# Optimization experiments

Measured on AMD Instinct MI355X. Metric: run time of the kernel, lower is better.

The kernel has to match this reference:

```python
import jax, jax.numpy as jnp
import numpy as np

V, E, H, S = 50257, 1024, 1024, 2048


def setup_inputs() -> dict:
    key = jax.random.key(0)
    ks = jax.random.split(key, 24)
    def n(k, shape, s=0.02):
        return jax.random.normal(k, shape, dtype=jnp.float32) * s
    inp = {
        "x": jax.random.normal(ks[0], (1, E), dtype=jnp.float32),
        "encoder_outputs": jax.random.normal(ks[1], (S, 2 * H), dtype=jnp.float32),
        "sentence": jax.random.randint(ks[2], (S,), 0, V, dtype=jnp.int32).at[0].set(7),
        "prev_probs": jax.random.uniform(ks[3], (V + S,), dtype=jnp.float32),
        "h0": n(ks[4], (1, H), 1.0),
        "c0": n(ks[5], (1, H), 1.0),
        "attn_W": n(ks[6], (S, 2 * H)), "attn_b": jnp.zeros((S,), jnp.float32),
        "comb_W": n(ks[7], (H, 2 * H)), "comb_b": jnp.zeros((H,), jnp.float32),
        "Ws_W": n(ks[8], (H, 2 * H)), "Ws_b": jnp.zeros((H,), jnp.float32),
        "Wo_W": n(ks[9], (V, H)), "Wo_b": jnp.zeros((V,), jnp.float32),
        "Wc_W": n(ks[10], (H, 2 * H)), "Wc_b": jnp.zeros((H,), jnp.float32),
        "W_ih": n(ks[11], (4 * H, E + 2 * H)), "W_hh": n(ks[12], (4 * H, H)),
        "b_ih": jnp.zeros((4 * H,), jnp.float32), "b_hh": jnp.zeros((4 * H,), jnp.float32),
        "prev_word": 7,
    }
    return inp


def reference(x, encoder_outputs, sentence, prev_probs, h0, c0,
              attn_W, attn_b, comb_W, comb_b, Ws_W, Ws_b,
              Wo_W, Wo_b, Wc_W, Wc_b, W_ih, W_hh, b_ih, b_hh, prev_word):
    xe, h, c = x[0], h0[0], c0[0]            # [E], [H], [H]
    # attentive read: attention over encoder positions, then combine to [H]
    att_logits = jnp.concatenate([xe, h]) @ attn_W.T + attn_b      # [S]
    attn_w = jax.nn.softmax(att_logits)
    ctx = attn_w @ encoder_outputs                                 # [2H]
    attentive = ctx @ comb_W.T + comb_b                            # [H]
    # selective read (copy mechanism): positions where sentence == prev_word
    probs_c = prev_probs[V:]                                       # [S]
    rho = jnp.where(sentence == prev_word, probs_c, 0.0)
    rho = rho / (rho.sum() + 1e-9)
    selective = (rho @ encoder_outputs) @ Ws_W.T + Ws_b            # [H]
    # single LSTM step (PyTorch gate order i,f,g,o)
    lstm_in = jnp.concatenate([xe, selective, attentive])          # [E+2H]
    gates = lstm_in @ W_ih.T + b_ih + h @ W_hh.T + b_hh            # [4H]
    i, f, g, o = jnp.split(gates, 4)
    c1 = jax.nn.sigmoid(f) * c + jax.nn.sigmoid(i) * jnp.tanh(g)
    h1 = jax.nn.sigmoid(o) * jnp.tanh(c1)                          # [H]
    # generate + copy scores, joint softmax
    score_g = h1 @ Wo_W.T + Wo_b                                   # [V]
    score_c = jnp.tanh(encoder_outputs @ Wc_W.T + Wc_b) @ h1       # [S]
    probs = jax.nn.softmax(jnp.concatenate([score_g, score_c]))    # [V+S]
    return probs, h1[None, :], c1[None, :]
```

## Files before the change

kernel.cpp:

```cpp
#include <hip/hip_runtime.h>
#include <hip/hip_bf16.h>
#include <math.h>

#define VV 50257
#define EE 1024
#define HH 1024
#define SS 2048
#define VS (VV + SS)

#define OFF_LOGA   0
#define OFF_ATTW   2048
#define OFF_RHO    4096
#define OFF_CTX    6144
#define OFF_SEL    8192
#define OFF_LSTMIN 10240
#define OFF_GATES  13312
#define OFF_H1     17408
#define OFF_LOG    18432
#define OFF_MS     70784
#define OFF_LS     70912
#define OFF_G      71040
#define OFF_T0     71168
#define OFF_T1     (71168 + 2048*1024)

typedef __attribute__((ext_vector_type(8))) short bf16x8;
typedef __attribute__((ext_vector_type(4))) float f32x4;

__device__ inline float wave_reduce(float v) {
    #pragma unroll
    for (int off = 32; off > 0; off >>= 1) v += __shfl_down(v, off, 64);
    return v;
}

__device__ inline unsigned short f2bf(float f) {
    unsigned int u = __builtin_bit_cast(unsigned int, f);
    u += 0x7FFFu + ((u >> 16) & 1u);
    return (unsigned short)(u >> 16);
}

__global__ void k_attn_logits(const float* __restrict__ x, const float* __restrict__ h0,
                              const float* __restrict__ attn_W, const float* __restrict__ attn_b,
                              float* __restrict__ out) {
    int wave = (blockIdx.x * blockDim.x + threadIdx.x) >> 6;
    int lane = threadIdx.x & 63;
    if (wave >= SS) return;
    const float4* rp = (const float4*)(attn_W + (size_t)wave * 2048);
    float acc = 0.f;
    #pragma unroll
    for (int k = 0; k < 8; ++k) {
        int idx = lane + 64 * k;
        float4 w = rp[idx];
        int j = idx * 4;
        const float* cat = (j < 1024) ? (x + j) : (h0 + (j - 1024));
        acc += w.x * cat[0] + w.y * cat[1] + w.z * cat[2] + w.w * cat[3];
    }
    acc = wave_reduce(acc);
    if (lane == 0) out[wave] = acc + attn_b[wave];
}

__global__ void k_prep(const float* __restrict__ logits, const int* __restrict__ sentence,
                       const float* __restrict__ prev_probs, const int* __restrict__ prev_word,
                       const float* __restrict__ x,
                       float* __restrict__ attn_w, float* __restrict__ rho,
                       float* __restrict__ lstm_in, float* __restrict__ ctxsel) {
    __shared__ float red[256];
    int tid = threadIdx.x;
    for (int j = tid; j < 4096; j += 256) ctxsel[j] = 0.f;
    float m = -1e30f;
    for (int s = tid; s < SS; s += 256) m = fmaxf(m, logits[s]);
    red[tid] = m; __syncthreads();
    for (int o = 128; o > 0; o >>= 1) { if (tid < o) red[tid] = fmaxf(red[tid], red[tid + o]); __syncthreads(); }
    m = red[0]; __syncthreads();
    float sum = 0.f;
    for (int s = tid; s < SS; s += 256) sum += expf(logits[s] - m);
    red[tid] = sum; __syncthreads();
    for (int o = 128; o > 0; o >>= 1) { if (tid < o) red[tid] += red[tid + o]; __syncthreads(); }
    float inv = 1.f / red[0]; __syncthreads();
    for (int s = tid; s < SS; s += 256) attn_w[s] = expf(logits[s] - m) * inv;
    int pw = prev_word[0];
    float rsum = 0.f;
    for (int s = tid; s < SS; s += 256) rsum += (sentence[s] == pw) ? prev_probs[VV + s] : 0.f;
    red[tid] = rsum; __syncthreads();
    for (int o = 128; o > 0; o >>= 1) { if (tid < o) red[tid] += red[tid + o]; __syncthreads(); }
    float rinv = 1.f / (red[0] + 1e-9f); __syncthreads();
    for (int s = tid; s < SS; s += 256) rho[s] = ((sentence[s] == pw) ? prev_probs[VV + s] : 0.f) * rinv;
    for (int j = tid; j < EE; j += 256) lstm_in[j] = x[j];
}

__global__ void k_ctx(const float* __restrict__ enc, const float* __restrict__ attn_w,
                      const float* __restrict__ rho, float* __restrict__ ctx,
                      float* __restrict__ selctx) {
    int col4 = blockIdx.x * 256 + threadIdx.x;
    int s0 = blockIdx.y * 64;
    float4 a = {0.f, 0.f, 0.f, 0.f}, r = {0.f, 0.f, 0.f, 0.f};
    const float4* p = (const float4*)enc + (size_t)s0 * 512 + col4;
    #pragma unroll 4
    for (int i = 0; i < 64; ++i) {
        float4 v = p[(size_t)i * 512];
        float w = attn_w[s0 + i], q = rho[s0 + i];
        a.x += w * v.x; a.y += w * v.y; a.z += w * v.z; a.w += w * v.w;
        r.x += q * v.x; r.y += q * v.y; r.z += q * v.z; r.w += q * v.w;
    }
    int c = col4 * 4;
    atomicAdd(&ctx[c], a.x); atomicAdd(&ctx[c+1], a.y); atomicAdd(&ctx[c+2], a.z); atomicAdd(&ctx[c+3], a.w);
    atomicAdd(&selctx[c], r.x); atomicAdd(&selctx[c+1], r.y); atomicAdd(&selctx[c+2], r.z); atomicAdd(&selctx[c+3], r.w);
}

__global__ void k_comb(const float* __restrict__ ctx, const float* __restrict__ selctx,
                       const float* __restrict__ comb_W, const float* __restrict__ comb_b,
                       const float* __restrict__ Ws_W, const float* __restrict__ Ws_b,
                       float* __restrict__ lstm_in) {
    int wave = (blockIdx.x * blockDim.x + threadIdx.x) >> 6;
    int lane = threadIdx.x & 63;
    if (wave >= 2048) return;
    bool sel = wave >= 1024;
    int i = sel ? wave - 1024 : wave;
    const float4* rp = (const float4*)((sel ? Ws_W : comb_W) + (size_t)i * 2048);
    const float4* vp = (const float4*)(sel ? selctx : ctx);
    float acc = 0.f;
    #pragma unroll
    for (int k = 0; k < 8; ++k) {
        int idx = lane + 64 * k;
        float4 w = rp[idx]; float4 v = vp[idx];
        acc += w.x * v.x + w.y * v.y + w.z * v.z + w.w * v.w;
    }
    acc = wave_reduce(acc);
    if (lane == 0) lstm_in[sel ? (1024 + i) : (2048 + i)] = acc + (sel ? Ws_b[i] : comb_b[i]);
}

__global__ __launch_bounds__(256) void k_gates_gemm(
        const float* __restrict__ lstm_in, const float* __restrict__ h0,
        const float* __restrict__ W_ih, const float* __restrict__ W_hh,
        const float* __restrict__ b_ih, const float* __restrict__ b_hh,
        float* __restrict__ gates,
        const float* __restrict__ A,
        const float* __restrict__ B,
        float* __restrict__ T0, float* __restrict__ T1) {
    __shared__ unsigned short As[128 * 32];
    __shared__ unsigned short Bs[128 * 32];
    int tid = threadIdx.x;
    if (blockIdx.x < 1024) {
        int wave = (blockIdx.x * 256 + tid) >> 6;
        int lane = tid & 63;
        const float4* rp = (const float4*)(W_ih + (size_t)wave * 3072);
        const float4* vp = (const float4*)lstm_in;
        float acc = 0.f;
        #pragma unroll
        for (int k = 0; k < 12; ++k) {
            int idx = lane + 64 * k;
            float4 w = rp[idx]; float4 v = vp[idx];
            acc += w.x * v.x + w.y * v.y + w.z * v.z + w.w * v.w;
        }
        const float4* hp = (const float4*)(W_hh + (size_t)wave * 1024);
        const float4* h4 = (const float4*)h0;
        #pragma unroll
        for (int k = 0; k < 4; ++k) {
            int idx = lane + 64 * k;
            float4 w = hp[idx]; float4 v = h4[idx];
            acc += w.x * v.x + w.y * v.y + w.z * v.z + w.w * v.w;
        }
        acc = wave_reduce(acc);
        if (lane == 0) gates[wave] = acc + b_ih[wave] + b_hh[wave];
        return;
    }
    int gg = blockIdx.x - 1024;
    int sK = gg >> 7;
    int rem = gg & 127;
    int mbase = (rem >> 3) * 128;
    int nbase = (rem & 7) * 128;
    float* C = sK ? T1 : T0;
    int lane = tid & 63;
    int wid = tid >> 6;
    int wm = (wid >> 1) * 64;
    int wn = (wid & 1) * 64;
    int lrow = lane & 15;
    int lk = (lane >> 4) * 8;
    f32x4 acc[4][4] = {};
    int kbeg = sK * 1024;
    for (int k0 = kbeg; k0 < kbeg + 1024; k0 += 32) {
        #pragma unroll
        for (int i = 0; i < 4; ++i) {
            int fi = tid + 256 * i;
            int row = fi >> 3;
            int kg = fi & 7;
            float4 v = *(const float4*)(A + (size_t)(mbase + row) * 2048 + k0 + kg * 4);
            ushort4 a4 = { f2bf(v.x), f2bf(v.y), f2bf(v.z), f2bf(v.w) };
            *(ushort4*)(As + row * 32 + kg * 4) = a4;
            float4 w = *(const float4*)(B + (size_t)(nbase + row) * 2048 + k0 + kg * 4);
            ushort4 b4 = { f2bf(w.x), f2bf(w.y), f2bf(w.z), f2bf(w.w) };
            *(ushort4*)(Bs + row * 32 + kg * 4) = b4;
        }
        __syncthreads();
        bf16x8 af[4], bfr[4];
        #pragma unroll
        for (int t = 0; t < 4; ++t) {
            af[t]  = *(const bf16x8*)(As + (wm + t * 16 + lrow) * 32 + lk);
            bfr[t] = *(const bf16x8*)(Bs + (wn + t * 16 + lrow) * 32 + lk);
        }
        #pragma unroll
        for (int mt = 0; mt < 4; ++mt)
            #pragma unroll
            for (int nt = 0; nt < 4; ++nt)
                acc[mt][nt] = __builtin_amdgcn_mfma_f32_16x16x32_bf16(af[mt], bfr[nt], acc[mt][nt], 0, 0, 0);
        __syncthreads();
    }
    int crow0 = (lane >> 4) * 4;
    int ccol = lane & 15;
    #pragma unroll
    for (int mt = 0; mt < 4; ++mt)
        #pragma unroll
        for (int nt = 0; nt < 4; ++nt) {
            int col = nbase + wn + nt * 16 + ccol;
            #pragma unroll
            for (int r = 0; r < 4; ++r) {
                int row = mbase + wm + mt * 16 + crow0 + r;
                C[(size_t)row * 1024 + col] = acc[mt][nt][r];
            }
        }
}

__global__ void k_lstm(const float* __restrict__ gates, const float* __restrict__ c0,
                       float* __restrict__ out, float* __restrict__ h1ws) {
    int k = blockIdx.x * 256 + threadIdx.x;
    float ig = gates[k], fg = gates[1024 + k], gg = gates[2048 + k], og = gates[3072 + k];
    float si = 1.f / (1.f + expf(-ig));
    float sf = 1.f / (1.f + expf(-fg));
    float so = 1.f / (1.f + expf(-og));
    float c1 = sf * c0[k] + si * tanhf(gg);
    float h1 = so * tanhf(c1);
    out[VS + k] = h1;
    out[VS + 1024 + k] = c1;
    h1ws[k] = h1;
}

__global__ void k_scores(const float* __restrict__ Wo_W, const float* __restrict__ Wo_b,
                         const float* __restrict__ T0, const float* __restrict__ T1,
                         const float* __restrict__ Wc_b,
                         const float* __restrict__ h1, float* __restrict__ logits) {
    int wave = (blockIdx.x * blockDim.x + threadIdx.x) >> 6;
    int lane = threadIdx.x & 63;
    if (wave >= VS) return;
    const float4* hp = (const float4*)h1;
    float acc = 0.f;
    if (wave < VV) {
        const float4* rp = (const float4*)(Wo_W + (size_t)wave * 1024);
        #pragma unroll
        for (int k = 0; k < 4; ++k) {
            int idx = lane + 64 * k;
            float4 w = rp[idx]; float4 v = hp[idx];
            acc += w.x * v.x + w.y * v.y + w.z * v.z + w.w * v.w;
        }
        acc = wave_reduce(acc);
        if (lane == 0) logits[wave] = acc + Wo_b[wave];
    } else {
        int r = wave - VV;
        const float4* p0 = (const float4*)(T0 + (size_t)r * 1024);
        const float4* p1 = (const float4*)(T1 + (size_t)r * 1024);
        const float4* bp = (const float4*)Wc_b;
        #pragma unroll
        for (int k = 0; k < 4; ++k) {
            int idx = lane + 64 * k;
            float4 a0 = p0[idx]; float4 a1 = p1[idx]; float4 bb = bp[idx]; float4 v = hp[idx];
            acc += tanhf(a0.x + a1.x + bb.x) * v.x + tanhf(a0.y + a1.y + bb.y) * v.y
                 + tanhf(a0.z + a1.z + bb.z) * v.z + tanhf(a0.w + a1.w + bb.w) * v.w;
        }
        acc = wave_reduce(acc);
        if (lane == 0) logits[wave] = acc;
    }
}

__global__ void k_sm1(const float* __restrict__ logits, float* __restrict__ ms, float* __restrict__ ls) {
    __shared__ float rm[256], rl[256];
    int tid = threadIdx.x;
    float m = -1e30f, l = 0.f;
    for (int v = blockIdx.x * 256 + tid; v < VS; v += 128 * 256) {
        float x = logits[v];
        float nm = fmaxf(m, x);
        l = l * expf(m - nm) + expf(x - nm);
        m = nm;
    }
    rm[tid] = m; rl[tid] = l; __syncthreads();
    for (int o = 128; o > 0; o >>= 1) {
        if (tid < o) {
            float m2 = rm[tid + o], l2 = rl[tid + o];
            float nm = fmaxf(rm[tid], m2);
            rl[tid] = rl[tid] * expf(rm[tid] - nm) + l2 * expf(m2 - nm);
            rm[tid] = nm;
        }
        __syncthreads();
    }
    if (tid == 0) { ms[blockIdx.x] = rm[0]; ls[blockIdx.x] = rl[0]; }
}

__global__ void k_sm2(const float* __restrict__ ms, const float* __restrict__ ls, float* __restrict__ g) {
    __shared__ float rm[128], rl[128];
    int tid = threadIdx.x;
    rm[tid] = ms[tid]; rl[tid] = ls[tid]; __syncthreads();
    for (int o = 64; o > 0; o >>= 1) {
        if (tid < o) {
            float m2 = rm[tid + o], l2 = rl[tid + o];
            float nm = fmaxf(rm[tid], m2);
            rl[tid] = rl[tid] * expf(rm[tid] - nm) + l2 * expf(m2 - nm);
            rm[tid] = nm;
        }
        __syncthreads();
    }
    if (tid == 0) { g[0] = rm[0]; g[1] = 1.f / rl[0]; }
}

__global__ void k_sm3(const float* __restrict__ logits, const float* __restrict__ g,
                      float* __restrict__ out) {
    int v = blockIdx.x * 256 + threadIdx.x;
    if (v < VS) out[v] = expf(logits[v] - g[0]) * g[1];
}

extern "C" void kernel_launch(void* const* d_in, const int* in_sizes, int n_in,
                              void* d_out, int out_size, void* d_ws, size_t ws_size,
                              hipStream_t stream) {
    (void)in_sizes; (void)n_in; (void)out_size; (void)ws_size;
    const float* x          = (const float*)d_in[0];
    const float* enc        = (const float*)d_in[1];
    const int*   sentence   = (const int*)d_in[2];
    const float* prev_probs = (const float*)d_in[3];
    const float* h0         = (const float*)d_in[4];
    const float* c0         = (const float*)d_in[5];
    const float* attn_W     = (const float*)d_in[6];
    const float* attn_b     = (const float*)d_in[7];
    const float* comb_W     = (const float*)d_in[8];
    const float* comb_b     = (const float*)d_in[9];
    const float* Ws_W       = (const float*)d_in[10];
    const float* Ws_b       = (const float*)d_in[11];
    const float* Wo_W       = (const float*)d_in[12];
    const float* Wo_b       = (const float*)d_in[13];
    const float* Wc_W       = (const float*)d_in[14];
    const float* Wc_b       = (const float*)d_in[15];
    const float* W_ih       = (const float*)d_in[16];
    const float* W_hh       = (const float*)d_in[17];
    const float* b_ih       = (const float*)d_in[18];
    const float* b_hh       = (const float*)d_in[19];
    const int*   prev_word  = (const int*)d_in[20];
    float* ws  = (float*)d_ws;
    float* out = (float*)d_out;

    k_attn_logits<<<512, 256, 0, stream>>>(x, h0, attn_W, attn_b, ws + OFF_LOGA);
    k_prep<<<1, 256, 0, stream>>>(ws + OFF_LOGA, sentence, prev_probs, prev_word, x,
                                  ws + OFF_ATTW, ws + OFF_RHO, ws + OFF_LSTMIN, ws + OFF_CTX);
    k_ctx<<<dim3(2, 32), 256, 0, stream>>>(enc, ws + OFF_ATTW, ws + OFF_RHO,
                                           ws + OFF_CTX, ws + OFF_SEL);
    k_comb<<<512, 256, 0, stream>>>(ws + OFF_CTX, ws + OFF_SEL, comb_W, comb_b,
                                    Ws_W, Ws_b, ws + OFF_LSTMIN);
    k_gates_gemm<<<1280, 256, 0, stream>>>(ws + OFF_LSTMIN, h0, W_ih, W_hh, b_ih, b_hh,
                                           ws + OFF_GATES, enc, Wc_W,
                                           ws + OFF_T0, ws + OFF_T1);
    k_lstm<<<4, 256, 0, stream>>>(ws + OFF_GATES, c0, out, ws + OFF_H1);
    k_scores<<<13077, 256, 0, stream>>>(Wo_W, Wo_b, ws + OFF_T0, ws + OFF_T1, Wc_b,
                                        ws + OFF_H1, ws + OFF_LOG);
    k_sm1<<<128, 256, 0, stream>>>(ws + OFF_LOG, ws + OFF_MS, ws + OFF_LS);
    k_sm2<<<1, 128, 0, stream>>>(ws + OFF_MS, ws + OFF_LS, ws + OFF_G);
    k_sm3<<<205, 256, 0, stream>>>(ws + OFF_LOG, ws + OFF_G, out);
}
```

Baseline: 480.5 us.

## Fuse small kernels via last-block atomic counters and split ctx reduction finer

```diff
diff --git a/kernel.cpp b/kernel.cpp
--- a/kernel.cpp
+++ b/kernel.cpp
@@ -7,6 +7,7 @@
 #define HH 1024
 #define SS 2048
 #define VS (VV + SS)
+#define NSB 13077
 
 #define OFF_LOGA   0
 #define OFF_ATTW   2048
@@ -16,12 +17,13 @@
 #define OFF_LSTMIN 10240
 #define OFF_GATES  13312
 #define OFF_H1     17408
-#define OFF_LOG    18432
+#define OFF_CNT    18432
+#define OFF_LOG    18448
 #define OFF_MS     70784
-#define OFF_LS     70912
-#define OFF_G      71040
-#define OFF_T0     71168
-#define OFF_T1     (71168 + 2048*1024)
+#define OFF_LS     83968
+#define OFF_G      97152
+#define OFF_T0     97280
+#define OFF_T1     (97280 + 2097152)
 
 typedef __attribute__((ext_vector_type(8))) short bf16x8;
 typedef __attribute__((ext_vector_type(4))) float f32x4;
@@ -38,12 +40,17 @@
     return (unsigned short)(u >> 16);
 }
 
-__global__ void k_attn_logits(const float* __restrict__ x, const float* __restrict__ h0,
-                              const float* __restrict__ attn_W, const float* __restrict__ attn_b,
-                              float* __restrict__ out) {
-    int wave = (blockIdx.x * blockDim.x + threadIdx.x) >> 6;
-    int lane = threadIdx.x & 63;
-    if (wave >= SS) return;
+__global__ __launch_bounds__(256) void k_attn(
+        const float* __restrict__ x, const float* __restrict__ h0,
+        const float* __restrict__ attn_W, const float* __restrict__ attn_b,
+        float* __restrict__ loga, unsigned int* __restrict__ cnt,
+        const int* __restrict__ sentence, const float* __restrict__ prev_probs,
+        const int* __restrict__ prev_word,
+        float* __restrict__ attn_w, float* __restrict__ rho,
+        float* __restrict__ lstm_in, float* __restrict__ ctxsel) {
+    int tid = threadIdx.x;
+    int wave = (blockIdx.x * 256 + tid) >> 6;
+    int lane = tid & 63;
     const float4* rp = (const float4*)(attn_W + (size_t)wave * 2048);
     float acc = 0.f;
     #pragma unroll
@@ -55,28 +62,27 @@
         acc += w.x * cat[0] + w.y * cat[1] + w.z * cat[2] + w.w * cat[3];
     }
     acc = wave_reduce(acc);
-    if (lane == 0) out[wave] = acc + attn_b[wave];
-}
-
-__global__ void k_prep(const float* __restrict__ logits, const int* __restrict__ sentence,
-                       const float* __restrict__ prev_probs, const int* __restrict__ prev_word,
-                       const float* __restrict__ x,
-                       float* __restrict__ attn_w, float* __restrict__ rho,
-                       float* __restrict__ lstm_in, float* __restrict__ ctxsel) {
+    if (lane == 0) loga[wave] = acc + attn_b[wave];
+    __threadfence();
+    __syncthreads();
+    __shared__ unsigned int isLast;
+    if (tid == 0) isLast = (atomicAdd(cnt, 1u) == 511u) ? 1u : 0u;
+    __syncthreads();
+    if (!isLast) return;
+    __threadfence();
     __shared__ float red[256];
-    int tid = threadIdx.x;
     for (int j = tid; j < 4096; j += 256) ctxsel[j] = 0.f;
     float m = -1e30f;
-    for (int s = tid; s < SS; s += 256) m = fmaxf(m, logits[s]);
+    for (int s = tid; s < SS; s += 256) m = fmaxf(m, loga[s]);
     red[tid] = m; __syncthreads();
     for (int o = 128; o > 0; o >>= 1) { if (tid < o) red[tid] = fmaxf(red[tid], red[tid + o]); __syncthreads(); }
     m = red[0]; __syncthreads();
     float sum = 0.f;
-    for (int s = tid; s < SS; s += 256) sum += expf(logits[s] - m);
+    for (int s = tid; s < SS; s += 256) sum += expf(loga[s] - m);
     red[tid] = sum; __syncthreads();
     for (int o = 128; o > 0; o >>= 1) { if (tid < o) red[tid] += red[tid + o]; __syncthreads(); }
     float inv = 1.f / red[0]; __syncthreads();
-    for (int s = tid; s < SS; s += 256) attn_w[s] = expf(logits[s] - m) * inv;
+    for (int s = tid; s < SS; s += 256) attn_w[s] = expf(loga[s] - m) * inv;
     int pw = prev_word[0];
     float rsum = 0.f;
     for (int s = tid; s < SS; s += 256) rsum += (sentence[s] == pw) ? prev_probs[VV + s] : 0.f;
@@ -91,11 +97,11 @@
                       const float* __restrict__ rho, float* __restrict__ ctx,
                       float* __restrict__ selctx) {
     int col4 = blockIdx.x * 256 + threadIdx.x;
-    int s0 = blockIdx.y * 64;
+    int s0 = blockIdx.y * 16;
     float4 a = {0.f, 0.f, 0.f, 0.f}, r = {0.f, 0.f, 0.f, 0.f};
     const float4* p = (const float4*)enc + (size_t)s0 * 512 + col4;
-    #pragma unroll 4
-    for (int i = 0; i < 64; ++i) {
+    #pragma unroll
+    for (int i = 0; i < 16; ++i) {
         float4 v = p[(size_t)i * 512];
         float w = attn_w[s0 + i], q = rho[s0 + i];
         a.x += w * v.x; a.y += w * v.y; a.z += w * v.z; a.w += w * v.w;
@@ -132,7 +138,8 @@
         const float* __restrict__ lstm_in, const float* __restrict__ h0,
         const float* __restrict__ W_ih, const float* __restrict__ W_hh,
         const float* __restrict__ b_ih, const float* __restrict__ b_hh,
-        float* __restrict__ gates,
+        float* __restrict__ gates, unsigned int* __restrict__ cnt,
+        const float* __restrict__ c0, float* __restrict__ out, float* __restrict__ h1ws,
         const float* __restrict__ A,
         const float* __restrict__ B,
         float* __restrict__ T0, float* __restrict__ T1) {
@@ -161,6 +168,24 @@
         }
         acc = wave_reduce(acc);
         if (lane == 0) gates[wave] = acc + b_ih[wave] + b_hh[wave];
+        __threadfence();
+        __syncthreads();
+        __shared__ unsigned int isLast;
+        if (tid == 0) isLast = (atomicAdd(cnt, 1u) == 1023u) ? 1u : 0u;
+        __syncthreads();
+        if (!isLast) return;
+        __threadfence();
+        for (int k = tid; k < 1024; k += 256) {
+            float ig = gates[k], fg = gates[1024 + k], gg = gates[2048 + k], og = gates[3072 + k];
+            float si = 1.f / (1.f + expf(-ig));
+            float sf = 1.f / (1.f + expf(-fg));
+            float so = 1.f / (1.f + expf(-og));
+            float c1 = sf * c0[k] + si * tanhf(gg);
+            float h1 = so * tanhf(c1);
+            out[VS + k] = h1;
+            out[VS + 1024 + k] = c1;
+            h1ws[k] = h1;
+        }
         return;
     }
     int gg = blockIdx.x - 1024;
@@ -219,84 +244,76 @@
         }
 }
 
-__global__ void k_lstm(const float* __restrict__ gates, const float* __restrict__ c0,
-                       float* __restrict__ out, float* __restrict__ h1ws) {
-    int k = blockIdx.x * 256 + threadIdx.x;
-    float ig = gates[k], fg = gates[1024 + k], gg = gates[2048 + k], og = gates[3072 + k];
-    float si = 1.f / (1.f + expf(-ig));
-    float sf = 1.f / (1.f + expf(-fg));
-    float so = 1.f / (1.f + expf(-og));
-    float c1 = sf * c0[k] + si * tanhf(gg);
-    float h1 = so * tanhf(c1);
-    out[VS + k] = h1;
-    out[VS + 1024 + k] = c1;
-    h1ws[k] = h1;
-}
-
-__global__ void k_scores(const float* __restrict__ Wo_W, const float* __restrict__ Wo_b,
-                         const float* __restrict__ T0, const float* __restrict__ T1,
-                         const float* __restrict__ Wc_b,
-                         const float* __restrict__ h1, float* __restrict__ logits) {
-    int wave = (blockIdx.x * blockDim.x + threadIdx.x) >> 6;
-    int lane = threadIdx.x & 63;
-    if (wave >= VS) return;
+__global__ __launch_bounds__(256) void k_scores(
+        const float* __restrict__ Wo_W, const float* __restrict__ Wo_b,
+        const float* __restrict__ T0, const float* __restrict__ T1,
+        const float* __restrict__ Wc_b, const float* __restrict__ h1,
+        float* __restrict__ logits, float* __restrict__ ms, float* __restrict__ ls,
+        unsigned int* __restrict__ cnt, float* __restrict__ g) {
+    int tid = threadIdx.x;
+    int wid = tid >> 6;
+    int lane = tid & 63;
+    int wave = blockIdx.x * 4 + wid;
     const float4* hp = (const float4*)h1;
-    float acc = 0.f;
-    if (wave < VV) {
-        const float4* rp = (const float4*)(Wo_W + (size_t)wave * 1024);
-        #pragma unroll
-        for (int k = 0; k < 4; ++k) {
-            int idx = lane + 64 * k;
-            float4 w = rp[idx]; float4 v = hp[idx];
-            acc += w.x * v.x + w.y * v.y + w.z * v.z + w.w * v.w;
-        }
-        acc = wave_reduce(acc);
-        if (lane == 0) logits[wave] = acc + Wo_b[wave];
-    } else {
-        int r = wave - VV;
-        const float4* p0 = (const float4*)(T0 + (size_t)r * 1024);
-        const float4* p1 = (const float4*)(T1 + (size_t)r * 1024);
-        const float4* bp = (const float4*)Wc_b;
-        #pragma unroll
-        for (int k = 0; k < 4; ++k) {
-            int idx = lane + 64 * k;
-            float4 a0 = p0[idx]; float4 a1 = p1[idx]; float4 bb = bp[idx]; float4 v = hp[idx];
-            acc += tanhf(a0.x + a1.x + bb.x) * v.x + tanhf(a0.y + a1.y + bb.y) * v.y
-                 + tanhf(a0.z + a1.z + bb.z) * v.z + tanhf(a0.w + a1.w + bb.w) * v.w;
-        }
-        acc = wave_reduce(acc);
-        if (lane == 0) logits[wave] = acc;
-    }
-}
-
-__global__ void k_sm1(const float* __restrict__ logits, float* __restrict__ ms, float* __restrict__ ls) {
+    float logit = -1e30f;
+    if (wave < VS) {
+        float acc = 0.f;
+        if (wave < VV) {
+            const float4* rp = (const float4*)(Wo_W + (size_t)wave * 1024);
+            #pragma unroll
+            for (int k = 0; k < 4; ++k) {
+                int idx = lane + 64 * k;
+                float4 w = rp[idx]; float4 v = hp[idx];
+                acc += w.x * v.x + w.y * v.y + w.z * v.z + w.w * v.w;
+            }
+            acc = wave_reduce(acc);
+            if (lane == 0) { logit = acc + Wo_b[wave]; logits[wave] = logit; }
+        } else {
+            int r = wave - VV;
+            const float4* p0 = (const float4*)(T0 + (size_t)r * 1024);
+            const float4* p1 = (const float4*)(T1 + (size_t)r * 1024);
+            const float4* bp = (const float4*)Wc_b;
+            #pragma unroll
+            for (int k = 0; k < 4; ++k) {
+                int idx = lane + 64 * k;
+                float4 a0 = p0[idx]; float4 a1 = p1[idx]; float4 bb = bp[idx]; float4 v = hp[idx];
+                acc += tanhf(a0.x + a1.x + bb.x) * v.x + tanhf(a0.y + a1.y + bb.y) * v.y
+                     + tanhf(a0.z + a1.z + bb.z) * v.z + tanhf(a0.w + a1.w + bb.w) * v.w;
+            }
+            acc = wave_reduce(acc);
+            if (lane == 0) { logit = acc; logits[wave] = logit; }
+        }
+    }
+    __shared__ float smv[4];
+    __shared__ unsigned int isLast;
+    if (lane == 0) smv[wid] = logit;
+    __syncthreads();
+    if (tid == 0) {
+        float m = -1e30f, l = 0.f;
+        #pragma unroll
+        for (int i = 0; i < 4; ++i) {
+            float v = smv[i];
+            float nm = fmaxf(m, v);
+            l = l * expf(m - nm) + expf(v - nm);
+            m = nm;
+        }
+        ms[blockIdx.x] = m; ls[blockIdx.x] = l;
+        __threadfence();
+        isLast = (atomicAdd(cnt, 1u) == (unsigned)(NSB - 1)) ? 1u : 0u;
+    }
+    __syncthreads();
+    if (!isLast) return;
+    __threadfence();
     __shared__ float rm[256], rl[256];
-    int tid = threadIdx.x;
     float m = -1e30f, l = 0.f;
-    for (int v = blockIdx.x * 256 + tid; v < VS; v += 128 * 256) {
-        float x = logits[v];
-        float nm = fmaxf(m, x);
-        l = l * expf(m - nm) + expf(x - nm);
+    for (int i = tid; i < NSB; i += 256) {
+        float m2 = ms[i], l2 = ls[i];
+        float nm = fmaxf(m, m2);
+        l = l * expf(m - nm) + l2 * expf(m2 - nm);
         m = nm;
     }
     rm[tid] = m; rl[tid] = l; __syncthreads();
     for (int o = 128; o > 0; o >>= 1) {
-        if (tid < o) {
-            float m2 = rm[tid + o], l2 = rl[tid + o];
-            float nm = fmaxf(rm[tid], m2);
-            rl[tid] = rl[tid] * expf(rm[tid] - nm) + l2 * expf(m2 - nm);
-            rm[tid] = nm;
-        }
-        __syncthreads();
-    }
-    if (tid == 0) { ms[blockIdx.x] = rm[0]; ls[blockIdx.x] = rl[0]; }
-}
-
-__global__ void k_sm2(const float* __restrict__ ms, const float* __restrict__ ls, float* __restrict__ g) {
-    __shared__ float rm[128], rl[128];
-    int tid = threadIdx.x;
-    rm[tid] = ms[tid]; rl[tid] = ls[tid]; __syncthreads();
-    for (int o = 64; o > 0; o >>= 1) {
         if (tid < o) {
             float m2 = rm[tid + o], l2 = rl[tid + o];
             float nm = fmaxf(rm[tid], m2);
@@ -341,21 +358,21 @@
     const int*   prev_word  = (const int*)d_in[20];
     float* ws  = (float*)d_ws;
     float* out = (float*)d_out;
-
-    k_attn_logits<<<512, 256, 0, stream>>>(x, h0, attn_W, attn_b, ws + OFF_LOGA);
-    k_prep<<<1, 256, 0, stream>>>(ws + OFF_LOGA, sentence, prev_probs, prev_word, x,
-                                  ws + OFF_ATTW, ws + OFF_RHO, ws + OFF_LSTMIN, ws + OFF_CTX);
-    k_ctx<<<dim3(2, 32), 256, 0, stream>>>(enc, ws + OFF_ATTW, ws + OFF_RHO,
-                                           ws + OFF_CTX, ws + OFF_SEL);
+    unsigned int* cnt = (unsigned int*)(ws + OFF_CNT);
+
+    hipMemsetAsync(cnt, 0, 16, stream);
+    k_attn<<<512, 256, 0, stream>>>(x, h0, attn_W, attn_b, ws + OFF_LOGA, cnt + 0,
+                                    sentence, prev_probs, prev_word,
+                                    ws + OFF_ATTW, ws + OFF_RHO, ws + OFF_LSTMIN, ws + OFF_CTX);
+    k_ctx<<<dim3(2, 128), 256, 0, stream>>>(enc, ws + OFF_ATTW, ws + OFF_RHO,
+                                            ws + OFF_CTX, ws + OFF_SEL);
     k_comb<<<512, 256, 0, stream>>>(ws + OFF_CTX, ws + OFF_SEL, comb_W, comb_b,
                                     Ws_W, Ws_b, ws + OFF_LSTMIN);
     k_gates_gemm<<<1280, 256, 0, stream>>>(ws + OFF_LSTMIN, h0, W_ih, W_hh, b_ih, b_hh,
-                                           ws + OFF_GATES, enc, Wc_W,
-                                           ws + OFF_T0, ws + OFF_T1);
-    k_lstm<<<4, 256, 0, stream>>>(ws + OFF_GATES, c0, out, ws + OFF_H1);
-    k_scores<<<13077, 256, 0, stream>>>(Wo_W, Wo_b, ws + OFF_T0, ws + OFF_T1, Wc_b,
-                                        ws + OFF_H1, ws + OFF_LOG);
-    k_sm1<<<128, 256, 0, stream>>>(ws + OFF_LOG, ws + OFF_MS, ws + OFF_LS);
-    k_sm2<<<1, 128, 0, stream>>>(ws + OFF_MS, ws + OFF_LS, ws + OFF_G);
+                                           ws + OFF_GATES, cnt + 1, c0, out, ws + OFF_H1,
+                                           enc, Wc_W, ws + OFF_T0, ws + OFF_T1);
+    k_scores<<<NSB, 256, 0, stream>>>(Wo_W, Wo_b, ws + OFF_T0, ws + OFF_T1, Wc_b,
+                                      ws + OFF_H1, ws + OFF_LOG,
+                                      ws + OFF_MS, ws + OFF_LS, cnt + 2, ws + OFF_G);
     k_sm3<<<205, 256, 0, stream>>>(ws + OFF_LOG, ws + OFF_G, out);
 }
```

New measurement: 1.214 ms. 2.53x slower.
